# Kernel optimization log

Measured on AMD Instinct MI355X. Metric: run time of the kernel, lower is better.

Reference implementation:

```python
import jax, jax.numpy as jnp
import numpy as np

L, B, E, H = 512, 4, 512, 8
D = E // H  # head_dim = 64


def setup_inputs() -> dict:
    key = jax.random.key(0)
    ks = jax.random.split(key, 7)
    query = jax.random.normal(ks[0], (L, B, E), dtype=jnp.float32)
    relation_k = jax.random.normal(ks[1], (B, L, L, D), dtype=jnp.float32)
    relation_v = jax.random.normal(ks[2], (B, L, L, D), dtype=jnp.float32)
    # xavier-uniform-ish scale for the fused QKV projection
    lim = float(np.sqrt(6.0 / (3 * E + E)))
    in_proj_weight = jax.random.uniform(ks[3], (3 * E, E), jnp.float32, -lim, lim)
    in_proj_bias = jnp.zeros((3 * E,), jnp.float32)
    lim_o = float(np.sqrt(1.0 / E))
    out_proj_weight = jax.random.uniform(ks[4], (E, E), jnp.float32, -lim_o, lim_o)
    out_proj_bias = jnp.zeros((E,), jnp.float32)
    return {
        "query": query,
        "relation_k": relation_k,
        "relation_v": relation_v,
        "in_proj_weight": in_proj_weight,
        "in_proj_bias": in_proj_bias,
        "out_proj_weight": out_proj_weight,
        "out_proj_bias": out_proj_bias,
    }


def reference(query, relation_k, relation_v, in_proj_weight, in_proj_bias,
              out_proj_weight, out_proj_bias):
    # query == key == value (qkv_same path), shape (L, B, E)
    scaling = float(D) ** -0.5
    qkv = query @ in_proj_weight.T + in_proj_bias          # (L, B, 3E)
    q, k, v = jnp.split(qkv, 3, axis=-1)                   # each (L, B, E)
    q = q * scaling

    def to_bhld(t):  # (L, B, E) -> (B, H, L, D)
        return t.reshape(L, B, H, D).transpose(1, 2, 0, 3)

    q, k, v = to_bhld(q), to_bhld(k), to_bhld(v)

    # content scores
    scores = jnp.einsum('bhid,bhjd->bhij', q, k)           # (B, H, L, L)

    # relation_k term: torch does a flat .view of (B*H, L, L, D) -> (B*H*L, D, L)
    # which is a row-major REINTERPRETATION (not a transpose). Replicate via reshape:
    rk = relation_k.reshape(B, L, D, L)                    # per-(b,i) block (L*D,) -> (D, L)
    scores = scores + jnp.einsum('bhid,bidj->bhij', q, rk)

    w = jax.nn.softmax(scores, axis=-1)
    w = jnp.where(jnp.isnan(w), jnp.zeros_like(w), w)      # NaN guard as in original

    out = jnp.einsum('bhij,bhjd->bhid', w, v)              # (B, H, L, D)
    # relation_v term: (B*H*L, 1, L) @ (B*H*L, L, D) -> per-query weighted relation values
    out = out + jnp.einsum('bhij,bijd->bhid', w, relation_v)

    out = out.transpose(2, 0, 1, 3).reshape(L, B, E)       # (B,H,L,D) -> (L,B,E)
    return out @ out_proj_weight.T + out_proj_bias
```

## Files before the change

### kernel.cpp

```cpp
#include <hip/hip_runtime.h>
#include <hip/hip_fp16.h>
#include <stdint.h>


typedef short short8 __attribute__((ext_vector_type(8)));
typedef float f32x4 __attribute__((ext_vector_type(4)));
typedef unsigned short u16x4 __attribute__((ext_vector_type(4)));

static __device__ __forceinline__ uint16_t f2bf(float f) {
  uint32_t u = __float_as_uint(f);
  uint32_t r = (u + 0x7FFFu + ((u >> 16) & 1u)) >> 16;
  return (uint16_t)r;
}
static __device__ __forceinline__ float bf2f(uint16_t h) {
  return __uint_as_float(((uint32_t)h) << 16);
}
static __device__ __forceinline__ short8 ld8(const uint16_t* p) {
  return *(const short8*)p;
}
#define MFMA(a, b, c) __builtin_amdgcn_mfma_f32_16x16x32_bf16((a), (b), (c), 0, 0, 0)

__global__ __launch_bounds__(256) void k_conv_all(
    const float* __restrict__ in_w, const float* __restrict__ query,
    const float* __restrict__ out_w, uint16_t* __restrict__ w_hi,
    uint16_t* __restrict__ w_lo, uint16_t* __restrict__ a_hi,
    uint16_t* __restrict__ a_lo, uint16_t* __restrict__ wo_bf) {
  int e = (blockIdx.x * 256 + threadIdx.x) * 4;
  if (e < 786432) {
    f32x4 v = *(const f32x4*)(in_w + e);
    u16x4 hi, lo;
#pragma unroll
    for (int k = 0; k < 4; ++k) {
      hi[k] = f2bf(v[k]);
      lo[k] = f2bf(v[k] - bf2f(hi[k]));
    }
    *(u16x4*)(w_hi + e) = hi;
    *(u16x4*)(w_lo + e) = lo;
  } else if (e < 786432 + 1048576) {
    int o = e - 786432;
    f32x4 v = *(const f32x4*)(query + o);
    u16x4 hi, lo;
#pragma unroll
    for (int k = 0; k < 4; ++k) {
      hi[k] = f2bf(v[k]);
      lo[k] = f2bf(v[k] - bf2f(hi[k]));
    }
    *(u16x4*)(a_hi + o) = hi;
    *(u16x4*)(a_lo + o) = lo;
  } else {
    int o = e - 1835008;
    f32x4 v = *(const f32x4*)(out_w + o);
    u16x4 hi;
#pragma unroll
    for (int k = 0; k < 4; ++k) hi[k] = f2bf(v[k]);
    *(u16x4*)(wo_bf + o) = hi;
  }
}

__global__ __launch_bounds__(256) void k_inproj(
    const uint16_t* __restrict__ a_hi, const uint16_t* __restrict__ a_lo,
    const uint16_t* __restrict__ w_hi, const uint16_t* __restrict__ w_lo,
    const float* __restrict__ bias, float* __restrict__ q_s,
    uint16_t* __restrict__ q_bf, uint16_t* __restrict__ k_bf,
    uint16_t* __restrict__ v_bf) {
  const int wave = threadIdx.x >> 6, lane = threadIdx.x & 63;
  const int wr = wave >> 1, wc = wave & 1;
  const int rif = lane & 15, kg = lane >> 4;
  const int rbase = blockIdx.x * 64 + wr * 32;
  const int cbase = blockIdx.y * 64 + wc * 32;
  f32x4 acc[2][2] = {};
  for (int ks = 0; ks < 512; ks += 32) {
    int kofs = ks + kg * 8;
    short8 aH[2], aL[2], bH[2], bL[2];
#pragma unroll
    for (int m = 0; m < 2; ++m) {
      size_t idx = (size_t)(rbase + m * 16 + rif) * 512 + kofs;
      aH[m] = ld8(a_hi + idx);
      aL[m] = ld8(a_lo + idx);
    }
#pragma unroll
    for (int n = 0; n < 2; ++n) {
      size_t idx = (size_t)(cbase + n * 16 + rif) * 512 + kofs;
      bH[n] = ld8(w_hi + idx);
      bL[n] = ld8(w_lo + idx);
    }
#pragma unroll
    for (int m = 0; m < 2; ++m)
#pragma unroll
      for (int n = 0; n < 2; ++n) {
        acc[m][n] = MFMA(aH[m], bH[n], acc[m][n]);
        acc[m][n] = MFMA(aH[m], bL[n], acc[m][n]);
        acc[m][n] = MFMA(aL[m], bH[n], acc[m][n]);
      }
  }
#pragma unroll
  for (int m = 0; m < 2; ++m)
#pragma unroll
    for (int n = 0; n < 2; ++n)
#pragma unroll
      for (int r = 0; r < 4; ++r) {
        int row = rbase + m * 16 + kg * 4 + r;
        int col = cbase + n * 16 + rif;
        float val = acc[m][n][r] + bias[col];
        int l = row >> 2, b = row & 3;
        int sel = col >> 9, h = (col >> 6) & 7, d = col & 63;
        size_t oidx = ((size_t)(b * 8 + h) * 512 + l) * 64 + d;
        if (sel == 0) {
          val *= 0.125f;
          q_s[oidx] = val;
          q_bf[oidx] = f2bf(val);
        } else if (sel == 1) {
          k_bf[oidx] = f2bf(val);
        } else {
          v_bf[oidx] = f2bf(val);
        }
      }
}

__global__ __launch_bounds__(256) void k_scores(const uint16_t* __restrict__ q_bf,
                                                const uint16_t* __restrict__ k_bf,
                                                __half* __restrict__ scores) {
  const int bh = blockIdx.x;
  const uint16_t* qb = q_bf + (size_t)bh * 512 * 64;
  const uint16_t* kb = k_bf + (size_t)bh * 512 * 64;
  const int wave = threadIdx.x >> 6, lane = threadIdx.x & 63;
  const int wr = wave >> 1, wc = wave & 1;
  const int rif = lane & 15, kg = lane >> 4;
  const int ibase = blockIdx.y * 64 + wr * 32;
  const int jbase = blockIdx.z * 64 + wc * 32;
  f32x4 acc[2][2] = {};
#pragma unroll
  for (int ks = 0; ks < 64; ks += 32) {
    int kofs = ks + kg * 8;
    short8 A[2], Bb[2];
#pragma unroll
    for (int m = 0; m < 2; ++m) A[m] = ld8(qb + (size_t)(ibase + m * 16 + rif) * 64 + kofs);
#pragma unroll
    for (int n = 0; n < 2; ++n) Bb[n] = ld8(kb + (size_t)(jbase + n * 16 + rif) * 64 + kofs);
#pragma unroll
    for (int m = 0; m < 2; ++m)
#pragma unroll
      for (int n = 0; n < 2; ++n) acc[m][n] = MFMA(A[m], Bb[n], acc[m][n]);
  }
  __half* sc = scores + (size_t)bh * 512 * 512;
#pragma unroll
  for (int m = 0; m < 2; ++m)
#pragma unroll
    for (int n = 0; n < 2; ++n)
#pragma unroll
      for (int r = 0; r < 4; ++r)
        sc[(size_t)(ibase + m * 16 + kg * 4 + r) * 512 + (jbase + n * 16 + rif)] =
            __float2half(acc[m][n][r]);
}

__global__ __launch_bounds__(256) void k_mega(
    const float* __restrict__ relation_k, const float* __restrict__ relation_v,
    const float* __restrict__ q_s, const __half* __restrict__ scores,
    uint16_t* __restrict__ wprob, uint16_t* __restrict__ rv_bf) {
  __shared__ float qv[64 * 8];
  __shared__ float sx[8 * 512];
  __shared__ uint16_t wlds[8 * 512];
  const int b = blockIdx.x >> 9, i = blockIdx.x & 511;
  const int t = threadIdx.x;
  const int wave = t >> 6, lane = t & 63;
  for (int e = t; e < 512; e += 256) {
    int h = e >> 6, d = e & 63;
    qv[d * 8 + h] = q_s[(((size_t)b * 8 + h) * 512 + i) * 64 + d];
  }
  __syncthreads();
  const int quad = t & 127, rep = t >> 7;
  const int j0 = quad * 4;
  const float* rkb = relation_k + ((size_t)b * 512 + i) * 32768;
  {
    f32x4 acc[8] = {};
    for (int dd = 0; dd < 32; ++dd) {
      int d = rep * 32 + dd;
      f32x4 rk4 = *(const f32x4*)(rkb + (size_t)d * 512 + j0);
      f32x4 q0 = *(const f32x4*)&qv[d * 8];
      f32x4 q1 = *(const f32x4*)&qv[d * 8 + 4];
#pragma unroll
      for (int h = 0; h < 4; ++h)
#pragma unroll
        for (int c = 0; c < 4; ++c) acc[h][c] += q0[h] * rk4[c];
#pragma unroll
      for (int h = 0; h < 4; ++h)
#pragma unroll
        for (int c = 0; c < 4; ++c) acc[4 + h][c] += q1[h] * rk4[c];
    }
    if (rep == 1) {
#pragma unroll
      for (int h = 0; h < 8; ++h) *(f32x4*)&sx[h * 512 + j0] = acc[h];
    }
    __syncthreads();
    if (rep == 0) {
#pragma unroll
      for (int h = 0; h < 8; ++h) {
        f32x4 o = *(f32x4*)&sx[h * 512 + j0];
#pragma unroll
        for (int c = 0; c < 4; ++c) o[c] += acc[h][c];
        *(f32x4*)&sx[h * 512 + j0] = o;
      }
    }
  }
  __syncthreads();
  for (int hh = 0; hh < 2; ++hh) {
    int h = wave * 2 + hh;
    const __half* srow = scores + (((size_t)b * 8 + h) * 512 + i) * 512;
    float s[8], m = -1e30f;
#pragma unroll
    for (int jj = 0; jj < 8; ++jj) {
      int j = jj * 64 + lane;
      s[jj] = __half2float(srow[j]) + sx[h * 512 + j];
      m = fmaxf(m, s[jj]);
    }
    for (int o = 32; o > 0; o >>= 1) m = fmaxf(m, __shfl_xor(m, o));
    float ex[8], sum = 0.f;
#pragma unroll
    for (int jj = 0; jj < 8; ++jj) {
      ex[jj] = __expf(s[jj] - m);
      sum += ex[jj];
    }
    for (int o = 32; o > 0; o >>= 1) sum += __shfl_xor(sum, o);
    float r = 1.f / sum;
    uint16_t* wrow = wprob + (((size_t)b * 8 + h) * 512 + i) * 512;
#pragma unroll
    for (int jj = 0; jj < 8; ++jj) {
      int j = jj * 64 + lane;
      uint16_t wv = f2bf(ex[jj] * r);
      wrow[j] = wv;
      int ba = (h * 1024 + j * 2) ^ ((h & 7) << 4);
      *(uint16_t*)((char*)wlds + ba) = wv;
    }
  }
  __syncthreads();
  const int rif = lane & 15, kg = lane >> 4;
  const int dt = wave;
  const float* rvb = relation_v + ((size_t)b * 512 + i) * 32768;
  f32x4 acc2 = {};
  for (int ks = 0; ks < 16; ++ks) {
    short8 A = {};
    if (rif < 8) {
      int ba = (rif * 1024 + (ks * 32 + kg * 8) * 2) ^ ((rif & 7) << 4);
      A = *(const short8*)((const char*)wlds + ba);
    }
    uint16_t tb[8];
#pragma unroll
    for (int e = 0; e < 8; ++e)
      tb[e] = f2bf(rvb[(size_t)(ks * 32 + kg * 8 + e) * 64 + dt * 16 + rif]);
    short8 Bb = *(const short8*)tb;
    acc2 = MFMA(A, Bb, acc2);
  }
  if (kg < 2) {
#pragma unroll
    for (int r = 0; r < 4; ++r) {
      int h = kg * 4 + r;
      int d = dt * 16 + rif;
      rv_bf[((size_t)i * 4 + b) * 512 + h * 64 + d] = f2bf(acc2[r]);
    }
  }
}

__global__ __launch_bounds__(256) void k_pv(const uint16_t* __restrict__ w_bf,
                                            const uint16_t* __restrict__ v_bf,
                                            uint16_t* __restrict__ pv_bf) {
  const int bh = blockIdx.x;
  const int b = bh >> 3, h = bh & 7;
  const uint16_t* wb = w_bf + (size_t)bh * 512 * 512;
  const uint16_t* vb = v_bf + (size_t)bh * 512 * 64;
  const int wave = threadIdx.x >> 6, lane = threadIdx.x & 63;
  const int wr = wave >> 1, wc = wave & 1;
  const int rif = lane & 15, kg = lane >> 4;
  const int ibase = blockIdx.y * 64 + wr * 32;
  const int dbase = wc * 32;
  f32x4 acc[2][2] = {};
  for (int ks = 0; ks < 512; ks += 32) {
    int kofs = ks + kg * 8;
    short8 A[2], Bb[2];
#pragma unroll
    for (int m = 0; m < 2; ++m) A[m] = ld8(wb + (size_t)(ibase + m * 16 + rif) * 512 + kofs);
#pragma unroll
    for (int n = 0; n < 2; ++n) {
      uint16_t tb[8];
#pragma unroll
      for (int e = 0; e < 8; ++e) tb[e] = vb[(size_t)(kofs + e) * 64 + dbase + n * 16 + rif];
      Bb[n] = *(const short8*)tb;
    }
#pragma unroll
    for (int m = 0; m < 2; ++m)
#pragma unroll
      for (int n = 0; n < 2; ++n) acc[m][n] = MFMA(A[m], Bb[n], acc[m][n]);
  }
#pragma unroll
  for (int m = 0; m < 2; ++m)
#pragma unroll
    for (int n = 0; n < 2; ++n)
#pragma unroll
      for (int r = 0; r < 4; ++r) {
        int i = ibase + m * 16 + kg * 4 + r;
        int d = dbase + n * 16 + rif;
        pv_bf[((size_t)i * 4 + b) * 512 + h * 64 + d] = f2bf(acc[m][n][r]);
      }
}

__global__ __launch_bounds__(256) void k_outproj(const uint16_t* __restrict__ rv_a,
                                                 const uint16_t* __restrict__ pv_a,
                                                 const uint16_t* __restrict__ wo_bf,
                                                 const float* __restrict__ bias,
                                                 float* __restrict__ out) {
  const int wave = threadIdx.x >> 6, lane = threadIdx.x & 63;
  const int wr = wave >> 1, wc = wave & 1;
  const int rif = lane & 15, kg = lane >> 4;
  const int rbase = blockIdx.x * 64 + wr * 32;
  const int cbase = blockIdx.y * 64 + wc * 32;
  f32x4 acc[2][2] = {};
  for (int ks = 0; ks < 512; ks += 32) {
    int kofs = ks + kg * 8;
    short8 A[2], Bb[2];
#pragma unroll
    for (int m = 0; m < 2; ++m) {
      size_t idx = (size_t)(rbase + m * 16 + rif) * 512 + kofs;
      short8 p = ld8(pv_a + idx);
      short8 rr = ld8(rv_a + idx);
      uint16_t tb[8];
#pragma unroll
      for (int e = 0; e < 8; ++e)
        tb[e] = f2bf(bf2f((uint16_t)p[e]) + bf2f((uint16_t)rr[e]));
      A[m] = *(const short8*)tb;
    }
#pragma unroll
    for (int n = 0; n < 2; ++n) Bb[n] = ld8(wo_bf + (size_t)(cbase + n * 16 + rif) * 512 + kofs);
#pragma unroll
    for (int m = 0; m < 2; ++m)
#pragma unroll
      for (int n = 0; n < 2; ++n) acc[m][n] = MFMA(A[m], Bb[n], acc[m][n]);
  }
#pragma unroll
  for (int m = 0; m < 2; ++m)
#pragma unroll
    for (int n = 0; n < 2; ++n)
#pragma unroll
      for (int r = 0; r < 4; ++r) {
        int row = rbase + m * 16 + kg * 4 + r;
        int col = cbase + n * 16 + rif;
        out[(size_t)row * 512 + col] = acc[m][n][r] + bias[col];
      }
}

extern "C" void kernel_launch(void* const* d_in, const int* in_sizes, int n_in,
                              void* d_out, int out_size, void* d_ws, size_t ws_size,
                              hipStream_t stream) {
  const float* query = (const float*)d_in[0];
  const float* relation_k = (const float*)d_in[1];
  const float* relation_v = (const float*)d_in[2];
  const float* in_w = (const float*)d_in[3];
  const float* in_b = (const float*)d_in[4];
  const float* out_w = (const float*)d_in[5];
  const float* out_b = (const float*)d_in[6];
  float* out = (float*)d_out;
  char* ws = (char*)d_ws;

  uint16_t* a_hi  = (uint16_t*)(ws + 0);
  uint16_t* a_lo  = (uint16_t*)(ws + 2097152);
  uint16_t* w_hi  = (uint16_t*)(ws + 4194304);
  uint16_t* w_lo  = (uint16_t*)(ws + 5767168);
  uint16_t* wo_bf = (uint16_t*)(ws + 7340032);
  float*    q_s   = (float*)   (ws + 7864320);
  uint16_t* q_bf  = (uint16_t*)(ws + 12058624);
  uint16_t* k_bf  = (uint16_t*)(ws + 14155776);
  uint16_t* v_bf  = (uint16_t*)(ws + 16252928);
  uint16_t* rv_bf = (uint16_t*)(ws + 18350080);
  uint16_t* pv_bf = (uint16_t*)(ws + 20447232);
  uint16_t* wprob = (uint16_t*)(ws + 22544384);
  __half*   sc_h  = (__half*)  (ws + 39321600);

  k_conv_all<<<dim3(2048), 256, 0, stream>>>(in_w, query, out_w, w_hi, w_lo, a_hi, a_lo, wo_bf);
  k_inproj<<<dim3(32, 24), 256, 0, stream>>>(a_hi, a_lo, w_hi, w_lo, in_b, q_s, q_bf, k_bf, v_bf);
  k_scores<<<dim3(32, 8, 8), 256, 0, stream>>>(q_bf, k_bf, sc_h);
  k_mega<<<dim3(2048), 256, 0, stream>>>(relation_k, relation_v, q_s, sc_h, wprob, rv_bf);
  k_pv<<<dim3(32, 8), 256, 0, stream>>>(wprob, v_bf, pv_bf);
  k_outproj<<<dim3(32, 8), 256, 0, stream>>>(rv_bf, pv_bf, wo_bf, out_b, out);
}
```

Before: 204.7 us.

## Replace relation_v MFMA with coalesced FMA, alias LDS, raise occupancy hint

In k_mega, the relation_v weighted sum no longer uses a half-empty MFMA fed by strided per-element fp32 loads and bf16 conversions. Each wave now streams a contiguous block of 128 relation_v rows with lane-coalesced loads, does scalar FMAs against bf16 probabilities stored in LDS in j-major order, and reduces the per-wave partials through shared memory. LDS usage shrinks by aliasing the qv and probability buffers and reusing sx for the partials. A min-blocks-per-SM launch bound of 6 is added, and the relation_k loop is unrolled by 4 so more loads are in flight. The aim is better memory-level parallelism on this bandwidth-bound kernel, at the cost of more VALU work and extra barriers.

```diff
diff --git a/kernel.cpp b/kernel.cpp
--- a/kernel.cpp
+++ b/kernel.cpp
@@ -153,13 +153,15 @@
             __float2half(acc[m][n][r]);
 }
 
-__global__ __launch_bounds__(256) void k_mega(
+__global__ __launch_bounds__(256, 6) void k_mega(
     const float* __restrict__ relation_k, const float* __restrict__ relation_v,
     const float* __restrict__ q_s, const __half* __restrict__ scores,
     uint16_t* __restrict__ wprob, uint16_t* __restrict__ rv_bf) {
-  __shared__ float qv[64 * 8];
-  __shared__ float sx[8 * 512];
-  __shared__ uint16_t wlds[8 * 512];
+  __shared__ float sx[4096];
+  __shared__ uint8_t regB[8192];
+  float* qv = (float*)regB;
+  uint16_t* pb = (uint16_t*)regB;
+  float* partials = sx;
   const int b = blockIdx.x >> 9, i = blockIdx.x & 511;
   const int t = threadIdx.x;
   const int wave = t >> 6, lane = t & 63;
@@ -172,20 +174,25 @@
   const int j0 = quad * 4;
   const float* rkb = relation_k + ((size_t)b * 512 + i) * 32768;
   {
+    const float* rkd = rkb + (size_t)rep * 32 * 512 + j0;
     f32x4 acc[8] = {};
-    for (int dd = 0; dd < 32; ++dd) {
-      int d = rep * 32 + dd;
-      f32x4 rk4 = *(const f32x4*)(rkb + (size_t)d * 512 + j0);
-      f32x4 q0 = *(const f32x4*)&qv[d * 8];
-      f32x4 q1 = *(const f32x4*)&qv[d * 8 + 4];
-#pragma unroll
-      for (int h = 0; h < 4; ++h)
-#pragma unroll
-        for (int c = 0; c < 4; ++c) acc[h][c] += q0[h] * rk4[c];
-#pragma unroll
-      for (int h = 0; h < 4; ++h)
-#pragma unroll
-        for (int c = 0; c < 4; ++c) acc[4 + h][c] += q1[h] * rk4[c];
+    for (int dd = 0; dd < 32; dd += 4) {
+      f32x4 kv[4];
+#pragma unroll
+      for (int u = 0; u < 4; ++u) kv[u] = *(const f32x4*)(rkd + (size_t)(dd + u) * 512);
+#pragma unroll
+      for (int u = 0; u < 4; ++u) {
+        int d = rep * 32 + dd + u;
+        f32x4 q0 = *(const f32x4*)&qv[d * 8];
+        f32x4 q1 = *(const f32x4*)&qv[d * 8 + 4];
+#pragma unroll
+        for (int h = 0; h < 4; ++h)
+#pragma unroll
+          for (int c = 0; c < 4; ++c) {
+            acc[h][c] += q0[h] * kv[u][c];
+            acc[4 + h][c] += q1[h] * kv[u][c];
+          }
+      }
     }
     if (rep == 1) {
 #pragma unroll
@@ -228,35 +235,42 @@
       int j = jj * 64 + lane;
       uint16_t wv = f2bf(ex[jj] * r);
       wrow[j] = wv;
-      int ba = (h * 1024 + j * 2) ^ ((h & 7) << 4);
-      *(uint16_t*)((char*)wlds + ba) = wv;
+      pb[j * 8 + h] = wv;
     }
   }
   __syncthreads();
-  const int rif = lane & 15, kg = lane >> 4;
-  const int dt = wave;
-  const float* rvb = relation_v + ((size_t)b * 512 + i) * 32768;
-  f32x4 acc2 = {};
-  for (int ks = 0; ks < 16; ++ks) {
-    short8 A = {};
-    if (rif < 8) {
-      int ba = (rif * 1024 + (ks * 32 + kg * 8) * 2) ^ ((rif & 7) << 4);
-      A = *(const short8*)((const char*)wlds + ba);
-    }
-    uint16_t tb[8];
-#pragma unroll
-    for (int e = 0; e < 8; ++e)
-      tb[e] = f2bf(rvb[(size_t)(ks * 32 + kg * 8 + e) * 64 + dt * 16 + rif]);
-    short8 Bb = *(const short8*)tb;
-    acc2 = MFMA(A, Bb, acc2);
-  }
-  if (kg < 2) {
-#pragma unroll
-    for (int r = 0; r < 4; ++r) {
-      int h = kg * 4 + r;
-      int d = dt * 16 + rif;
-      rv_bf[((size_t)i * 4 + b) * 512 + h * 64 + d] = f2bf(acc2[r]);
-    }
+  {
+    const float* rvb = relation_v + ((size_t)b * 512 + i) * 32768;
+    float acc[8] = {};
+    const int jb = wave * 128;
+    for (int jj = 0; jj < 128; jj += 4) {
+      int j = jb + jj;
+      float r0 = rvb[(size_t)(j + 0) * 64 + lane];
+      float r1 = rvb[(size_t)(j + 1) * 64 + lane];
+      float r2 = rvb[(size_t)(j + 2) * 64 + lane];
+      float r3 = rvb[(size_t)(j + 3) * 64 + lane];
+      short8 w0 = *(const short8*)&pb[(j + 0) * 8];
+      short8 w1 = *(const short8*)&pb[(j + 1) * 8];
+      short8 w2 = *(const short8*)&pb[(j + 2) * 8];
+      short8 w3 = *(const short8*)&pb[(j + 3) * 8];
+#pragma unroll
+      for (int h = 0; h < 8; ++h) {
+        acc[h] += bf2f((uint16_t)w0[h]) * r0;
+        acc[h] += bf2f((uint16_t)w1[h]) * r1;
+        acc[h] += bf2f((uint16_t)w2[h]) * r2;
+        acc[h] += bf2f((uint16_t)w3[h]) * r3;
+      }
+    }
+    __syncthreads();
+#pragma unroll
+    for (int h = 0; h < 8; ++h) partials[(wave * 8 + h) * 64 + lane] = acc[h];
+  }
+  __syncthreads();
+  for (int e = t; e < 512; e += 256) {
+    int h = e >> 6, d = e & 63;
+    float s = partials[(0 * 8 + h) * 64 + d] + partials[(1 * 8 + h) * 64 + d] +
+              partials[(2 * 8 + h) * 64 + d] + partials[(3 * 8 + h) * 64 + d];
+    rv_bf[((size_t)i * 4 + b) * 512 + h * 64 + d] = f2bf(s);
   }
 }
 
```

New measurement: 225.3 us. 1.1x slower.
